# Performance work log

Hardware: AMD Instinct MI355X
Metric: run time of the kernel (lower is better)

Reference implementation:

```python
import jax, jax.numpy as jnp
import numpy as np

TOP_K = 48
NUM_RBF = 16
MAX_REL = 32  # max_relative_feature
B, L = 2, 3072

# atom order in stacked tensor: N=0, Ca=1, C=2, O=3, Cb=4
_PAIRS = np.array([
    (0, 0), (2, 2), (3, 3), (4, 4), (1, 0), (1, 2), (1, 3), (1, 4),
    (0, 2), (0, 3), (0, 4), (4, 2), (4, 3), (3, 2), (0, 1), (2, 1),
    (3, 1), (4, 1), (2, 0), (3, 0), (4, 0), (2, 4), (3, 4), (2, 3)], dtype=np.int32)


def _rbf(D):
    # D [..., ] -> [..., NUM_RBF]
    mu = jnp.linspace(2.0, 22.0, NUM_RBF)
    sigma = (22.0 - 2.0) / NUM_RBF
    return jnp.exp(-(((D[..., None] - mu) / sigma) ** 2))


def setup_inputs() -> dict:
    key = jax.random.key(0)
    ks = jax.random.split(key, 8)
    X = jax.random.normal(ks[0], (B, L, 4, 3), dtype=jnp.float32) * 3.0
    mask = jnp.ones((B, L), dtype=jnp.float32)
    R_idx = jnp.sort(jax.random.randint(ks[1], (B, L), 0, 6144), axis=-1)
    chain_labels = jax.random.randint(ks[2], (B, L), 0, 4)
    pos_W = jax.random.normal(ks[3], (2 * MAX_REL + 2, 16), dtype=jnp.float32) * 0.1
    pos_b = jax.random.normal(ks[4], (16,), dtype=jnp.float32) * 0.02
    edge_W = jax.random.normal(ks[5], (16 + 25 * NUM_RBF, 128), dtype=jnp.float32) * 0.05
    ln_gamma = jnp.ones((128,), dtype=jnp.float32)
    ln_beta = jnp.zeros((128,), dtype=jnp.float32)
    return {"X": X, "mask": mask, "R_idx": R_idx, "chain_labels": chain_labels,
            "pos_W": pos_W, "pos_b": pos_b, "edge_W": edge_W,
            "ln_gamma": ln_gamma, "ln_beta": ln_beta}


def reference(X, mask, R_idx, chain_labels, pos_W, pos_b, edge_W, ln_gamma, ln_beta):
    # virtual Cb construction
    bvec = X[:, :, 1, :] - X[:, :, 0, :]
    cvec = X[:, :, 2, :] - X[:, :, 1, :]
    avec = jnp.cross(bvec, cvec)
    Ca = X[:, :, 1, :]
    Cb = -0.58273431 * avec + 0.56802827 * bvec - 0.54067466 * cvec + Ca
    atoms = jnp.stack([X[:, :, 0, :], Ca, X[:, :, 2, :], X[:, :, 3, :], Cb], axis=2)  # [B,L,5,3]

    # masked pairwise Ca distances + k smallest neighbors
    mask2d = mask[:, :, None] * mask[:, None, :]                        # [B,L,L]
    dX = Ca[:, :, None, :] - Ca[:, None, :, :]
    D = mask2d * jnp.sqrt(jnp.sum(dX ** 2, axis=-1) + 1e-6)
    D_max = jnp.max(D, axis=-1, keepdims=True)
    D_adjust = D + (1.0 - mask2d) * D_max
    k = min(TOP_K, X.shape[1])
    neg_vals, E_idx = jax.lax.top_k(-D_adjust, k)                       # [B,L,K]
    D_neighbors = -neg_vals

    # gather neighbor atom coords once: [B,L,K,5,3]
    atoms_nb = jax.vmap(lambda a, i: a[i])(atoms, E_idx)

    # 24 remaining atom-pair distances, restricted to neighbors (same math as
    # full cdist + gather since dist is computed per (i, E_idx[i,j]) pair)
    ai, bi = _PAIRS[:, 0], _PAIRS[:, 1]
    diff = atoms[:, :, None, ai, :] - atoms_nb[:, :, :, bi, :]          # [B,L,K,24,3]
    D24 = jnp.sqrt(jnp.sum(diff ** 2, axis=-1) + 1e-6)                  # [B,L,K,24]

    D_all = jnp.concatenate([D_neighbors[..., None], D24], axis=-1)    # [B,L,K,25]
    RBF_all = _rbf(D_all).reshape(D_all.shape[:3] + (25 * NUM_RBF,))   # [B,L,K,400]

    # positional encodings on neighbor offsets
    offset = R_idx[:, :, None] - R_idx[:, None, :]
    offset = jnp.take_along_axis(offset, E_idx, axis=2)                 # [B,L,K]
    same_chain = (chain_labels[:, :, None] - chain_labels[:, None, :] == 0).astype(jnp.int32)
    E_chains = jnp.take_along_axis(same_chain, E_idx, axis=2)           # [B,L,K]
    d = jnp.clip(offset + MAX_REL, 0, 2 * MAX_REL) * E_chains + (1 - E_chains) * (2 * MAX_REL + 1)
    E_positional = pos_W[d] + pos_b                                     # one-hot @ W == row gather

    E = jnp.concatenate([E_positional, RBF_all], axis=-1)              # [B,L,K,416]
    E = E @ edge_W                                                      # [B,L,K,128]
    mu = jnp.mean(E, axis=-1, keepdims=True)
    var = jnp.mean((E - mu) ** 2, axis=-1, keepdims=True)
    E = (E - mu) / jnp.sqrt(var + 1e-5) * ln_gamma + ln_beta
    return E, E_idx
```

## Files before the change

### kernel.cpp

```cpp
#include <hip/hip_runtime.h>
#include <hip/hip_bf16.h>
#include <stdint.h>
#include <math.h>

#define B_   2
#define L_   3072
#define K_   48
#define FDIM 416
#define NOUT 128
#define FRS8 424
#define NLUT 1920

__device__ const unsigned char PAIRC[24] = {
    0, 18, 27, 36, 8, 10, 11, 12, 2, 3, 4, 34, 35, 26,
    1, 17, 25, 33, 16, 24, 32, 20, 28, 19
};

typedef __attribute__((ext_vector_type(4))) float f32x4;

__global__ __launch_bounds__(256) void k_prep(const float* __restrict__ X,
                                              const float* __restrict__ mask,
                                              const float* __restrict__ edgeW,
                                              float* __restrict__ atoms,
                                              float* __restrict__ CaA4,
                                              unsigned char* __restrict__ Wt8,
                                              uint4* __restrict__ LUT)
{
    const int bid = blockIdx.x;
    if (bid < 52) {
        int idx4 = bid * 256 + threadIdx.x;
        int b = idx4 * 4;
        int lhi = (b >> 3) & 3;
        int l15 = (b >> 5) & 15;
        int nt  = (b >> 9) & 7;
        int kt  = b >> 12;
        int n = (nt >> 1) * 32 + 2 * l15 + (nt & 1);
        int kbase = kt * 32 + lhi * 8 + (b & 7);
        float v0 = edgeW[(kbase + 0) * NOUT + n];
        float v1 = edgeW[(kbase + 1) * NOUT + n];
        float v2 = edgeW[(kbase + 2) * NOUT + n];
        float v3 = edgeW[(kbase + 3) * NOUT + n];
        int w = __builtin_amdgcn_cvt_pk_fp8_f32(v0, v1, 0, false);
        w = __builtin_amdgcn_cvt_pk_fp8_f32(v2, v3, w, true);
        ((unsigned int*)Wt8)[idx4] = (unsigned int)w;
    } else if (bid < 60) {
        int e = (bid - 52) * 256 + threadIdx.x;
        if (e >= NLUT) return;
        float D = (float)e * 0.015625f;
        float z = (D - 2.0f) * 0.8f;
        unsigned int u[4];
        #pragma unroll
        for (int p = 0; p < 4; ++p) {
            float e0 = __expf(-(z * z)); z -= 1.0666667f;
            float e1 = __expf(-(z * z)); z -= 1.0666667f;
            float e2 = __expf(-(z * z)); z -= 1.0666667f;
            float e3 = __expf(-(z * z)); z -= 1.0666667f;
            int w = __builtin_amdgcn_cvt_pk_fp8_f32(e0, e1, 0, false);
            w = __builtin_amdgcn_cvt_pk_fp8_f32(e2, e3, w, true);
            u[p] = (unsigned int)w;
        }
        LUT[e] = make_uint4(u[0], u[1], u[2], u[3]);
    } else {
        int row = (bid - 60) * 256 + threadIdx.x;
        if (row >= B_ * L_) return;
        const float* x = X + row * 12;
        float nx = x[0], ny = x[1], nz = x[2];
        float cax = x[3], cay = x[4], caz = x[5];
        float cx = x[6], cy = x[7], cz = x[8];
        float ox = x[9], oy = x[10], oz = x[11];
        float bx = cax - nx, by = cay - ny, bz = caz - nz;
        float vx = cx - cax, vy = cy - cay, vz = cz - caz;
        float axv = by * vz - bz * vy;
        float ayv = bz * vx - bx * vz;
        float azv = bx * vy - by * vx;
        float cbx = -0.58273431f * axv + 0.56802827f * bx - 0.54067466f * vx + cax;
        float cby = -0.58273431f * ayv + 0.56802827f * by - 0.54067466f * vy + cay;
        float cbz = -0.58273431f * azv + 0.56802827f * bz - 0.54067466f * vz + caz;
        float* A = atoms + row * 16;
        A[0] = nx;  A[1] = ny;  A[2] = nz;
        A[3] = cax; A[4] = cay; A[5] = caz;
        A[6] = cx;  A[7] = cy;  A[8] = cz;
        A[9] = ox;  A[10] = oy; A[11] = oz;
        A[12] = cbx; A[13] = cby; A[14] = cbz;
        A[15] = 0.f;
        float4 c4 = make_float4(cax, cay, caz, mask[row]);
        *(float4*)(CaA4 + row * 4) = c4;
    }
}

__global__ __launch_bounds__(256) void k_topk(const float* __restrict__ CaA4,
                                              int* __restrict__ eidx,
                                              float* __restrict__ dnb,
                                              float* __restrict__ out_eidx_f)
{
    __shared__ __align__(16) unsigned int SH[3072];
    unsigned int* hist  = SH;
    unsigned int* candJ = SH + 2048;
    unsigned long long* candK = (unsigned long long*)SH;
    __shared__ unsigned int swave[4];
    __shared__ int sP;
    __shared__ unsigned int sCnt;

    const int row = blockIdx.x;
    const int b = row / L_;
    const int tid = threadIdx.x;
    const int lane = tid & 63;
    const int wv = tid >> 6;

    #pragma unroll
    for (int i = 0; i < 8; ++i) hist[tid + 256 * i] = 0;
    if (tid == 0) sCnt = 0;

    const float4 me = *(const float4*)(CaA4 + row * 4);
    const float4* Cb = (const float4*)(CaA4 + (size_t)b * L_ * 4);
    __syncthreads();

    unsigned int bits[12];
    #pragma unroll
    for (int m = 0; m < 12; ++m) {
        int j = tid + 256 * m;
        float4 nb = Cb[j];
        float dx = me.x - nb.x;
        float dy = me.y - nb.y;
        float dz = me.z - nb.z;
        float s = fmaf(dz, dz, fmaf(dy, dy, dx * dx)) + 1e-6f;
        bool live = (me.w * nb.w) != 0.0f;
        bits[m] = live ? __float_as_uint(s) : 0x7F800000u;
        atomicAdd(&hist[bits[m] >> 20], 1u);
    }
    __syncthreads();

    unsigned int loc[8];
    unsigned int s = 0;
    #pragma unroll
    for (int i = 0; i < 8; ++i) { loc[i] = hist[tid * 8 + i]; s += loc[i]; }
    unsigned int sc = s;
    #pragma unroll
    for (int off = 1; off < 64; off <<= 1) {
        unsigned int o = __shfl_up(sc, off);
        if (lane >= off) sc += o;
    }
    if (lane == 63) swave[wv] = sc;
    __syncthreads();
    unsigned int base = 0;
    #pragma unroll
    for (int w = 0; w < 4; ++w) if (w < wv) base += swave[w];
    unsigned int cum = base + sc - s;
    #pragma unroll
    for (int i = 0; i < 8; ++i) {
        unsigned int c = loc[i];
        if (cum < K_ && cum + c >= K_) sP = tid * 8 + i;
        cum += c;
    }
    __syncthreads();
    const unsigned int Pth = (unsigned int)sP + 2;

    #pragma unroll
    for (int m = 0; m < 12; ++m) {
        if ((bits[m] >> 20) <= Pth) {
            unsigned int pos = atomicAdd(&sCnt, 1u);
            if (pos < 1024) candJ[pos] = (unsigned)(tid + 256 * m);
        }
    }
    __syncthreads();
    int cnt = (int)sCnt;
    if (cnt > 1024) cnt = 1024;

    const double cax = (double)me.x, cay = (double)me.y, caz = (double)me.z;
    for (int i = tid; i < cnt; i += 256) {
        int j = (int)candJ[i];
        float4 nb = Cb[j];
        double dx = cax - (double)nb.x;
        double dy = cay - (double)nb.y;
        double dz = caz - (double)nb.z;
        double ss = dx * dx;
        ss = ss + dy * dy;
        ss = ss + dz * dz;
        ss = ss + 1e-6;
        float v = (float)sqrt(ss);
        candK[i] = ((unsigned long long)__float_as_uint(v) << 32) | (unsigned)j;
    }
    __syncthreads();

    if (cnt <= 64) {
        if (wv == 0) {
            unsigned long long k = (lane < cnt) ? candK[lane] : ~0ull;
            #pragma unroll
            for (int size = 2; size <= 64; size <<= 1) {
                #pragma unroll
                for (int stride = size >> 1; stride >= 1; stride >>= 1) {
                    unsigned long long o = __shfl_xor(k, stride);
                    bool low = (lane & stride) == 0;
                    bool up = (lane & size) == 0 || size == 64;
                    unsigned long long mn = k < o ? k : o;
                    unsigned long long mx = k < o ? o : k;
                    k = (low == up) ? mn : mx;
                }
            }
            if (lane < K_) {
                int gj = (int)(unsigned)(k & 0xffffffffu);
                eidx[row * K_ + lane] = gj;
                dnb[row * K_ + lane] = __uint_as_float((unsigned)(k >> 32));
                out_eidx_f[row * K_ + lane] = (float)gj;
            }
        }
    } else {
        int M2 = 128;
        while (M2 < cnt) M2 <<= 1;
        for (int i = cnt + tid; i < M2; i += 256) candK[i] = ~0ull;
        for (int size = 2; size <= M2; size <<= 1) {
            for (int stride = size >> 1; stride > 0; stride >>= 1) {
                __syncthreads();
                for (int i = tid; i < M2; i += 256) {
                    int p = i ^ stride;
                    if (p > i) {
                        unsigned long long a = candK[i];
                        unsigned long long c2 = candK[p];
                        bool up = ((i & size) == 0);
                        if ((a > c2) == up) { candK[i] = c2; candK[p] = a; }
                    }
                }
            }
        }
        __syncthreads();
        if (tid < K_) {
            unsigned long long g = candK[tid];
            int gj = (int)(unsigned)(g & 0xffffffffu);
            eidx[row * K_ + tid] = gj;
            dnb[row * K_ + tid] = __uint_as_float((unsigned)(g >> 32));
            out_eidx_f[row * K_ + tid] = (float)gj;
        }
    }
}

__global__ __launch_bounds__(256) void k_edge(const float* __restrict__ atoms,
                                              const int* __restrict__ eidx,
                                              const float* __restrict__ dnb,
                                              const int* __restrict__ Ridx,
                                              const int* __restrict__ chain,
                                              const float* __restrict__ posW,
                                              const float* __restrict__ posb,
                                              const unsigned char* __restrict__ Wt8,
                                              const uint4* __restrict__ LUT,
                                              const float* __restrict__ gamma,
                                              const float* __restrict__ beta,
                                              float* __restrict__ Eout)
{
    __shared__ __align__(16) unsigned char F8[K_ * FRS8];
    __shared__ __align__(16) float sOwn[16];
    __shared__ int   sE[K_];
    __shared__ float sDnb[K_];
    __shared__ int   sDpos[K_];
    __shared__ float Psum[K_][4];
    __shared__ float Psq[K_][4];
    __shared__ float sMu[K_];
    __shared__ float sInv[K_];

    const int row = blockIdx.x;
    const int b = row / L_;
    const int tid = threadIdx.x;

    if (tid < K_) {
        int j = eidx[row * K_ + tid];
        sE[tid] = j;
        sDnb[tid] = dnb[row * K_ + tid];
        int off = Ridx[row] - Ridx[b * L_ + j];
        int ch = (chain[row] == chain[b * L_ + j]) ? 1 : 0;
        sDpos[tid] = ch ? min(max(off + 32, 0), 64) : 65;
    } else if (tid < K_ + 4) {
        int part = tid - K_;
        *(float4*)(&sOwn[part * 4]) = *(const float4*)(atoms + (size_t)row * 16 + part * 4);
    }
    __syncthreads();

    if (tid < 240) {
        const int k = tid / 5;
        const int dd0 = tid - k * 5;
        const float* pj = atoms + ((size_t)b * L_ + sE[k]) * 16;
        unsigned char* Fk = F8 + k * FRS8;
        #pragma unroll
        for (int s5 = 0; s5 < 5; ++s5) {
            const int dd = dd0 + 5 * s5;
            float D;
            if (dd == 0) {
                D = sDnb[k];
            } else {
                int pr = PAIRC[dd - 1];
                int ai = pr >> 3, bi = pr & 7;
                float dx = sOwn[ai * 3 + 0] - pj[bi * 3 + 0];
                float dy = sOwn[ai * 3 + 1] - pj[bi * 3 + 1];
                float dz = sOwn[ai * 3 + 2] - pj[bi * 3 + 2];
                D = sqrtf(fmaf(dz, dz, fmaf(dy, dy, dx * dx)) + 1e-6f);
            }
            float Dc = fminf(D, 29.984375f);
            int idx = (int)fmaf(Dc, 64.0f, 0.5f);
            uint4 v = LUT[idx];
            *(uint4*)(Fk + 16 + dd * 16) = v;
        }
    }
    for (int s2 = tid; s2 < K_ * 16; s2 += 256) {
        int k = s2 >> 4, r = s2 & 15;
        float v = posW[sDpos[k] * 16 + r] + posb[r];
        int w = __builtin_amdgcn_cvt_pk_fp8_f32(v, v, 0, false);
        F8[k * FRS8 + r] = (unsigned char)(w & 0xff);
    }
    __syncthreads();

    const int lane = tid & 63;
    const int wv = tid >> 6;
    const int l15 = lane & 15;
    const int lhi = lane >> 4;

    f32x4 acc[3][2];
    #pragma unroll
    for (int mt = 0; mt < 3; ++mt)
        #pragma unroll
        for (int nn = 0; nn < 2; ++nn)
            acc[mt][nn] = (f32x4){0.f, 0.f, 0.f, 0.f};

    const unsigned char* wp = Wt8 + wv * 1024 + l15 * 32 + lhi * 8;
    long bc0 = *(const long*)(wp);
    long bc1 = *(const long*)(wp + 512);

    #pragma unroll 1
    for (int kt = 0; kt < 13; ++kt) {
        long bn0 = 0, bn1 = 0;
        if (kt < 12) {
            bn0 = *(const long*)(wp + (kt + 1) * 4096);
            bn1 = *(const long*)(wp + (kt + 1) * 4096 + 512);
        }
        const int k0 = kt * 32 + lhi * 8;
        long a0 = *(const long*)(F8 + (l15) * FRS8 + k0);
        long a1 = *(const long*)(F8 + (16 + l15) * FRS8 + k0);
        long a2 = *(const long*)(F8 + (32 + l15) * FRS8 + k0);
        acc[0][0] = __builtin_amdgcn_mfma_f32_16x16x32_fp8_fp8(a0, bc0, acc[0][0], 0, 0, 0);
        acc[0][1] = __builtin_amdgcn_mfma_f32_16x16x32_fp8_fp8(a0, bc1, acc[0][1], 0, 0, 0);
        acc[1][0] = __builtin_amdgcn_mfma_f32_16x16x32_fp8_fp8(a1, bc0, acc[1][0], 0, 0, 0);
        acc[1][1] = __builtin_amdgcn_mfma_f32_16x16x32_fp8_fp8(a1, bc1, acc[1][1], 0, 0, 0);
        acc[2][0] = __builtin_amdgcn_mfma_f32_16x16x32_fp8_fp8(a2, bc0, acc[2][0], 0, 0, 0);
        acc[2][1] = __builtin_amdgcn_mfma_f32_16x16x32_fp8_fp8(a2, bc1, acc[2][1], 0, 0, 0);
        bc0 = bn0;
        bc1 = bn1;
    }

    #pragma unroll
    for (int mt = 0; mt < 3; ++mt) {
        #pragma unroll
        for (int r = 0; r < 4; ++r) {
            float v0 = acc[mt][0][r], v1 = acc[mt][1][r];
            float sv = v0 + v1;
            float q = v0 * v0 + v1 * v1;
            #pragma unroll
            for (int off = 1; off < 16; off <<= 1) {
                sv += __shfl_xor(sv, off);
                q += __shfl_xor(q, off);
            }
            if (l15 == 0) {
                int er = mt * 16 + lhi * 4 + r;
                Psum[er][wv] = sv;
                Psq[er][wv] = q;
            }
        }
    }
    __syncthreads();

    if (tid < K_) {
        float sv = Psum[tid][0] + Psum[tid][1] + Psum[tid][2] + Psum[tid][3];
        float q  = Psq[tid][0] + Psq[tid][1] + Psq[tid][2] + Psq[tid][3];
        float mu = sv * (1.0f / 128.0f);
        float var = q * (1.0f / 128.0f) - mu * mu;
        sMu[tid] = mu;
        sInv[tid] = 1.0f / sqrtf(var + 1e-5f);
    }
    __syncthreads();

    const int c0p = wv * 32 + 2 * l15;
    float2 g2 = *(const float2*)(gamma + c0p);
    float2 b2 = *(const float2*)(beta + c0p);

    #pragma unroll
    for (int mt = 0; mt < 3; ++mt) {
        #pragma unroll
        for (int r = 0; r < 4; ++r) {
            int er = mt * 16 + lhi * 4 + r;
            float mu = sMu[er];
            float inv = sInv[er];
            float2 o;
            o.x = (acc[mt][0][r] - mu) * inv * g2.x + b2.x;
            o.y = (acc[mt][1][r] - mu) * inv * g2.y + b2.y;
            *(float2*)(Eout + ((size_t)row * K_ + er) * 128 + c0p) = o;
        }
    }
}

extern "C" void kernel_launch(void* const* d_in, const int* in_sizes, int n_in,
                              void* d_out, int out_size, void* d_ws, size_t ws_size,
                              hipStream_t stream) {
    const float* X     = (const float*)d_in[0];
    const float* mask  = (const float*)d_in[1];
    const int*   Ridx  = (const int*)d_in[2];
    const int*   chain = (const int*)d_in[3];
    const float* posW  = (const float*)d_in[4];
    const float* posb  = (const float*)d_in[5];
    const float* edgeW = (const float*)d_in[6];
    const float* gamma = (const float*)d_in[7];
    const float* beta  = (const float*)d_in[8];

    float* out   = (float*)d_out;
    float* Eout  = out;
    float* EidxF = out + (size_t)B_ * L_ * K_ * NOUT;

    float* atoms = (float*)d_ws;
    float* CaA4  = atoms + (size_t)B_ * L_ * 16;
    int*   eidx  = (int*)(CaA4 + (size_t)B_ * L_ * 4);
    float* dnb   = (float*)(eidx + (size_t)B_ * L_ * K_);
    unsigned char* Wt8 = (unsigned char*)(dnb + (size_t)B_ * L_ * K_);
    uint4* LUT   = (uint4*)(Wt8 + 53248);

    hipLaunchKernelGGL(k_prep, dim3(60 + (B_ * L_ + 255) / 256), dim3(256), 0, stream,
                       X, mask, edgeW, atoms, CaA4, Wt8, LUT);
    hipLaunchKernelGGL(k_topk, dim3(B_ * L_), dim3(256), 0, stream,
                       CaA4, eidx, dnb, EidxF);
    hipLaunchKernelGGL(k_edge, dim3(B_ * L_), dim3(256), 0, stream,
                       atoms, eidx, dnb, Ridx, chain, posW, posb, Wt8, LUT, gamma, beta, Eout);
}
```

Before: 116.5 us.

## Split per-edge distance LUT index computation into separate fully-parallel kernel

Moves the 25 per-edge atom-pair distance computations and their LUT index quantization out of k_edge into a new k_dist kernel. That kernel runs one thread per (edge, pair) and writes 16-bit indices to workspace. k_edge then only gathers LUT entries by index, which removes the scattered neighbor atom loads and the sqrt from its prologue. In exchange it adds a kernel launch and a global round-trip of about 14.7M bytes of indices.

```diff
diff --git a/kernel.cpp b/kernel.cpp
--- a/kernel.cpp
+++ b/kernel.cpp
@@ -233,9 +233,36 @@
     }
 }
 
-__global__ __launch_bounds__(256) void k_edge(const float* __restrict__ atoms,
+__global__ __launch_bounds__(256) void k_dist(const float* __restrict__ atoms,
                                               const int* __restrict__ eidx,
                                               const float* __restrict__ dnb,
+                                              unsigned short* __restrict__ Didx)
+{
+    int i = blockIdx.x * 256 + threadIdx.x;
+    int e = i / 25;
+    int dd = i - e * 25;
+    int row = e / K_;
+    int b = row / L_;
+    float D;
+    if (dd == 0) {
+        D = dnb[e];
+    } else {
+        int j = eidx[e];
+        int pr = PAIRC[dd - 1];
+        int ai = pr >> 3, bi = pr & 7;
+        const float* po = atoms + (size_t)row * 16;
+        const float* pj = atoms + ((size_t)(b * L_ + j)) * 16;
+        float dx = po[ai * 3 + 0] - pj[bi * 3 + 0];
+        float dy = po[ai * 3 + 1] - pj[bi * 3 + 1];
+        float dz = po[ai * 3 + 2] - pj[bi * 3 + 2];
+        D = sqrtf(fmaf(dz, dz, fmaf(dy, dy, dx * dx)) + 1e-6f);
+    }
+    float Dc = fminf(D, 29.984375f);
+    Didx[i] = (unsigned short)(int)fmaf(Dc, 64.0f, 0.5f);
+}
+
+__global__ __launch_bounds__(256) void k_edge(const unsigned short* __restrict__ Didx,
+                                              const int* __restrict__ eidx,
                                               const int* __restrict__ Ridx,
                                               const int* __restrict__ chain,
                                               const float* __restrict__ posW,
@@ -247,9 +274,6 @@
                                               float* __restrict__ Eout)
 {
     __shared__ __align__(16) unsigned char F8[K_ * FRS8];
-    __shared__ __align__(16) float sOwn[16];
-    __shared__ int   sE[K_];
-    __shared__ float sDnb[K_];
     __shared__ int   sDpos[K_];
     __shared__ float Psum[K_][4];
     __shared__ float Psq[K_][4];
@@ -262,39 +286,21 @@
 
     if (tid < K_) {
         int j = eidx[row * K_ + tid];
-        sE[tid] = j;
-        sDnb[tid] = dnb[row * K_ + tid];
         int off = Ridx[row] - Ridx[b * L_ + j];
         int ch = (chain[row] == chain[b * L_ + j]) ? 1 : 0;
         sDpos[tid] = ch ? min(max(off + 32, 0), 64) : 65;
-    } else if (tid < K_ + 4) {
-        int part = tid - K_;
-        *(float4*)(&sOwn[part * 4]) = *(const float4*)(atoms + (size_t)row * 16 + part * 4);
     }
     __syncthreads();
 
     if (tid < 240) {
         const int k = tid / 5;
         const int dd0 = tid - k * 5;
-        const float* pj = atoms + ((size_t)b * L_ + sE[k]) * 16;
+        const unsigned short* dptr = Didx + (size_t)row * (K_ * 25) + k * 25;
         unsigned char* Fk = F8 + k * FRS8;
         #pragma unroll
         for (int s5 = 0; s5 < 5; ++s5) {
             const int dd = dd0 + 5 * s5;
-            float D;
-            if (dd == 0) {
-                D = sDnb[k];
-            } else {
-                int pr = PAIRC[dd - 1];
-                int ai = pr >> 3, bi = pr & 7;
-                float dx = sOwn[ai * 3 + 0] - pj[bi * 3 + 0];
-                float dy = sOwn[ai * 3 + 1] - pj[bi * 3 + 1];
-                float dz = sOwn[ai * 3 + 2] - pj[bi * 3 + 2];
-                D = sqrtf(fmaf(dz, dz, fmaf(dy, dy, dx * dx)) + 1e-6f);
-            }
-            float Dc = fminf(D, 29.984375f);
-            int idx = (int)fmaf(Dc, 64.0f, 0.5f);
-            uint4 v = LUT[idx];
+            uint4 v = LUT[dptr[dd]];
             *(uint4*)(Fk + 16 + dd * 16) = v;
         }
     }
@@ -416,11 +422,14 @@
     float* dnb   = (float*)(eidx + (size_t)B_ * L_ * K_);
     unsigned char* Wt8 = (unsigned char*)(dnb + (size_t)B_ * L_ * K_);
     uint4* LUT   = (uint4*)(Wt8 + 53248);
+    unsigned short* Didx = (unsigned short*)(LUT + NLUT);
 
     hipLaunchKernelGGL(k_prep, dim3(60 + (B_ * L_ + 255) / 256), dim3(256), 0, stream,
                        X, mask, edgeW, atoms, CaA4, Wt8, LUT);
     hipLaunchKernelGGL(k_topk, dim3(B_ * L_), dim3(256), 0, stream,
                        CaA4, eidx, dnb, EidxF);
+    hipLaunchKernelGGL(k_dist, dim3(B_ * L_ * K_ * 25 / 256), dim3(256), 0, stream,
+                       atoms, eidx, dnb, Didx);
     hipLaunchKernelGGL(k_edge, dim3(B_ * L_), dim3(256), 0, stream,
-                       atoms, eidx, dnb, Ridx, chain, posW, posb, Wt8, LUT, gamma, beta, Eout);
+                       Didx, eidx, Ridx, chain, posW, posb, Wt8, LUT, gamma, beta, Eout);
 }
```

New measurement: 130.8 us. 12.3% more time.
